# Optimization experiments

Hardware: AMD Instinct MI355X
Metric: run time of the kernel (lower is better)

## Reference

```python
import jax, jax.numpy as jnp
import numpy as np

B, N, IN_DIM, DIM, HEADS, P = 4, 2048, 256, 512, 8, 16
DH = DIM // HEADS            # 64
SCALE = DH ** -0.5


def setup_inputs() -> dict:
    key = jax.random.key(0)
    ks = jax.random.split(key, 8)
    def w(k, shape, s=0.02):
        return jax.random.normal(k, shape, dtype=jnp.float32) * s
    return {
        "x": jax.random.normal(ks[0], (B, N, IN_DIM), dtype=jnp.float32),
        "w_qkv": w(ks[1], (IN_DIM, 3 * DIM)),
        "b_qkv": jnp.zeros((3 * DIM,), jnp.float32),
        "w_in": w(ks[2], (P, P)),
        "b_in": jnp.zeros((P,), jnp.float32),
        "w_out": w(ks[3], (P, P)),
        "b_out": jnp.zeros((P,), jnp.float32),
        "w_merge": w(ks[4], (DIM, DIM)),
        "b_merge": jnp.zeros((DIM,), jnp.float32),
        "w_proj": w(ks[5], (DIM + IN_DIM, DIM)),
        "b_proj": jnp.zeros((DIM,), jnp.float32),
        "H": 64,
        "W": 32,
    }


def reference(x, w_qkv, b_qkv, w_in, b_in, w_out, b_out,
              w_merge, b_merge, w_proj, b_proj, H, W):
    b, n, _ = x.shape
    qkv = x @ w_qkv + b_qkv                      # [b, n, 3*DIM]
    q, k, v = jnp.split(qkv, 3, axis=-1)
    def to_heads(t):
        return t.reshape(b, n, HEADS, DH).transpose(0, 2, 1, 3)  # [b, h, n, d]
    q, k, v = to_heads(q), to_heads(k), to_heads(v)
    # Original splits heads into h/v halves and runs two attentions, then
    # concats along the head axis. Softmax is per-head, so this is exactly
    # one batched multi-head attention with head order preserved.
    attn = jax.nn.softmax(jnp.einsum('bhnd,bhmd->bhnm', q, k) * SCALE, axis=-1)
    out = jnp.einsum('bhnm,bhmd->bhnd', attn, v)
    out = out.transpose(0, 2, 1, 3).reshape(b, n, DIM)
    out = out @ w_merge + b_merge
    # IBPP branch: view channels as [P, P] grid, linear-SiLU-linear on last dim
    xr = x.reshape(b, n, P, P)
    ib = jax.nn.silu(xr @ w_in + b_in) @ w_out + b_out
    ib = ib.reshape(b, n, IN_DIM)
    # proj (dropout p=0 -> identity)
    return jnp.concatenate([out, ib], axis=-1) @ w_proj + b_proj
```

## Files before the change

kernel.cpp:

```cpp
#include <hip/hip_runtime.h>


typedef unsigned short u16;
typedef unsigned int u32;
typedef __bf16 bf16x8 __attribute__((ext_vector_type(8)));
typedef u16 su16x8 __attribute__((ext_vector_type(8)));
typedef u16 su16x4 __attribute__((ext_vector_type(4)));
typedef u32 u32x4 __attribute__((ext_vector_type(4)));
typedef float f32x4 __attribute__((ext_vector_type(4)));
typedef float f32x16 __attribute__((ext_vector_type(16)));

__device__ __forceinline__ u16 f2bf(float f) {
  union { __bf16 h; u16 u; } v;
  v.h = (__bf16)f;
  return v.u;
}

__device__ __forceinline__ float fexp2(float x) {
#if __has_builtin(__builtin_amdgcn_exp2f)
  return __builtin_amdgcn_exp2f(x);
#else
  return __expf(x * 0.6931471805599453f);
#endif
}

__device__ __forceinline__ f32x4 zero4() {
  f32x4 v = {0.f, 0.f, 0.f, 0.f};
  return v;
}

__device__ __forceinline__ f32x4 mfma16(bf16x8 a, bf16x8 b, f32x4 c) {
  return __builtin_amdgcn_mfma_f32_16x16x32_bf16(a, b, c, 0, 0, 0);
}

__device__ __forceinline__ f32x16 mfma32(bf16x8 a, bf16x8 b, f32x16 c) {
  return __builtin_amdgcn_mfma_f32_32x32x16_bf16(a, b, c, 0, 0, 0);
}

__device__ __forceinline__ u32 pkbf(float a, float b) {
  u32 r;
  asm("v_cvt_pk_bf16_f32 %0, %1, %2" : "=v"(r) : "v"(a), "v"(b));
  return r;
}

__device__ __forceinline__ void swap32(u32& a, u32& b) {
  asm("v_permlane32_swap_b32 %0, %1" : "+v"(a), "+v"(b));
}

__device__ __forceinline__ bf16x8 mkfrag(u32 w0, u32 w1, u32 w2, u32 w3) {
  union { u32 u[4]; bf16x8 v; } x;
  x.u[0] = w0; x.u[1] = w1; x.u[2] = w2; x.u[3] = w3;
  return x.v;
}

__global__ __launch_bounds__(256) void prep_ib_kernel(
    const float* __restrict__ w_qkv, const float* __restrict__ w_merge,
    const float* __restrict__ w_proj, const float* __restrict__ b_merge,
    const float* __restrict__ b_proj, u16* __restrict__ wqkvT,
    u16* __restrict__ wptT, u16* __restrict__ wcombT, u16* __restrict__ wmb,
    float* __restrict__ biasc, const float* __restrict__ x,
    const float* __restrict__ w_in, const float* __restrict__ b_in,
    const float* __restrict__ w_out, const float* __restrict__ b_out,
    u16* __restrict__ xb, u16* __restrict__ catb) {
  __shared__ __align__(16) char smem[35456];
  int blk = blockIdx.x, tid = threadIdx.x;
  if (blk < 192) {
    const float* src;
    int lsrc, ldd, r0, c0;
    u16* dst;
    if (blk < 96) {
      src = w_qkv; lsrc = 1536; dst = wqkvT; ldd = 256;
      r0 = (blk & 3) * 64; c0 = (blk >> 2) * 64;
    } else if (blk < 160) {
      int b2 = blk - 96;
      src = w_proj; lsrc = 512; dst = wptT; ldd = 512;
      r0 = (b2 & 7) * 64; c0 = (b2 >> 3) * 64;
    } else {
      int b2 = blk - 160;
      src = w_proj + 512 * 512; lsrc = 512; dst = wcombT + 512; ldd = 768;
      r0 = (b2 & 3) * 64; c0 = (b2 >> 2) * 64;
    }
    u16* Ts = (u16*)smem;
    int rr = tid >> 4, cc4 = (tid & 15) * 4;
#pragma unroll
    for (int rep = 0; rep < 4; ++rep) {
      int r = rr + rep * 16;
      float4 v = *(const float4*)&src[(size_t)(r0 + r) * lsrc + c0 + cc4];
      su16x4 pk = {f2bf(v.x), f2bf(v.y), f2bf(v.z), f2bf(v.w)};
      *(su16x4*)&Ts[r * 68 + cc4] = pk;
    }
    __syncthreads();
    int c = tid & 63, seg = tid >> 6;
    u16 tmp[16];
#pragma unroll
    for (int k = 0; k < 16; ++k) tmp[k] = Ts[(seg * 16 + k) * 68 + c];
    *(su16x8*)&dst[(size_t)(c0 + c) * ldd + r0 + seg * 16] = *(su16x8*)tmp;
    *(su16x8*)&dst[(size_t)(c0 + c) * ldd + r0 + seg * 16 + 8] =
        *(su16x8*)(tmp + 8);
  } else if (blk < 256) {
    int b2 = blk - 192;
#pragma unroll
    for (int rep = 0; rep < 4; ++rep) {
      int i = b2 * 4096 + rep * 1024 + tid * 4;
      float4 v = *(const float4*)&w_merge[i];
      su16x4 pk = {f2bf(v.x), f2bf(v.y), f2bf(v.z), f2bf(v.w)};
      *(su16x4*)&wmb[i] = pk;
    }
  } else if (blk < 288) {
    int col0 = (blk - 256) * 16;
    float(*red)[17] = (float(*)[17])smem;
    int kr = tid >> 4, cc = tid & 15;
    float s = 0.f;
#pragma unroll 4
    for (int j = 0; j < 32; ++j) {
      int k = kr + j * 16;
      s += b_merge[k] * w_proj[(size_t)k * 512 + col0 + cc];
    }
    red[kr][cc] = s;
    __syncthreads();
    if (kr == 0) {
      float a = b_proj[col0 + cc];
#pragma unroll
      for (int t = 0; t < 16; ++t) a += red[t][cc];
      biasc[col0 + cc] = a;
    }
  } else {
    int ib = blk - 288;
    float* wi = (float*)smem;
    float* wo = (float*)(smem + 1024);
    float* bi = (float*)(smem + 2048);
    float* bo = (float*)(smem + 2112);
    float(*xs)[260] = (float(*)[260])(smem + 2176);
    float(*hs)[260] = (float(*)[260])(smem + 18816);
    wi[tid] = w_in[tid];
    wo[tid] = w_out[tid];
    if (tid < 16) { bi[tid] = b_in[tid]; bo[tid] = b_out[tid]; }
    size_t blkoff = (size_t)ib * 4096;
#pragma unroll
    for (int i = 0; i < 4; ++i) {
      int f = (tid + i * 256) * 4;
      float4 v = *(const float4*)&x[blkoff + f];
      int tok = f >> 8, p = f & 255;
      *(float4*)&xs[tok][p] = v;
      su16x4 pk = {f2bf(v.x), f2bf(v.y), f2bf(v.z), f2bf(v.w)};
      *(su16x4*)&xb[blkoff + f] = pk;
    }
    __syncthreads();
    int t = tid >> 4, p2 = tid & 15;
#pragma unroll
    for (int p1 = 0; p1 < 16; ++p1) {
      float a = bi[p2];
#pragma unroll
      for (int k = 0; k < 16; ++k) a += xs[t][p1 * 16 + k] * wi[k * 16 + p2];
      hs[t][p1 * 16 + p2] = a / (1.f + __expf(-a));
    }
    __syncthreads();
    size_t tok = (size_t)ib * 16 + t;
#pragma unroll
    for (int p1 = 0; p1 < 16; ++p1) {
      float o = bo[p2];
#pragma unroll
      for (int j = 0; j < 16; ++j) o += hs[t][p1 * 16 + j] * wo[j * 16 + p2];
      catb[tok * 768 + 512 + p1 * 16 + p2] = f2bf(o);
    }
  }
}

template <int TM, int TN, int WGM, int WGN, int OUTMODE>
__global__ __launch_bounds__(256) void gemm_bt(
    const u16* __restrict__ A, int lda, const u16* __restrict__ BT, int ldb,
    int kcount, const float* __restrict__ bias, void* __restrict__ Co, int ldc,
    int scaleQ) {
  constexpr int NROWS = TM + TN;
  constexpr int NLD = NROWS / 64;
  constexpr int MT = TM / WGM / 16;
  constexpr int NT = TN / WGN / 16;
  __shared__ __align__(16) u16 S[NROWS * 40];
  int tid = threadIdx.x;
  int lane = tid & 63, wave = tid >> 6;
  int c = lane & 15, g4 = lane >> 4;
  int m0 = blockIdx.y * TM, n0 = blockIdx.x * TN;
  int wm = (wave / WGN) * (TM / WGM), wn = (wave % WGN) * (TN / WGN);
  f32x4 acc[MT][NT];
#pragma unroll
  for (int a = 0; a < MT; ++a)
#pragma unroll
    for (int b = 0; b < NT; ++b) acc[a][b] = zero4();

  su16x8 pre[NLD];
#pragma unroll
  for (int t = 0; t < NLD; ++t) {
    int gsl = t * 256 + tid;
    int row = gsl >> 2, kg = gsl & 3;
    const u16* p = row < TM ? &A[(size_t)(m0 + row) * lda + kg * 8]
                            : &BT[(size_t)(n0 + row - TM) * ldb + kg * 8];
    pre[t] = *(const su16x8*)p;
  }

  for (int kb = 0; kb < kcount; kb += 32) {
    __syncthreads();
#pragma unroll
    for (int t = 0; t < NLD; ++t) {
      int gsl = t * 256 + tid;
      int row = gsl >> 2, kg = gsl & 3;
      *(su16x8*)&S[row * 40 + kg * 8] = pre[t];
    }
    __syncthreads();
    if (kb + 32 < kcount) {
#pragma unroll
      for (int t = 0; t < NLD; ++t) {
        int gsl = t * 256 + tid;
        int row = gsl >> 2, kg = gsl & 3;
        const u16* p =
            row < TM ? &A[(size_t)(m0 + row) * lda + kb + 32 + kg * 8]
                     : &BT[(size_t)(n0 + row - TM) * ldb + kb + 32 + kg * 8];
        pre[t] = *(const su16x8*)p;
      }
    }
    bf16x8 af[MT], bf[NT];
#pragma unroll
    for (int mt = 0; mt < MT; ++mt)
      af[mt] = *(const bf16x8*)&S[(wm + mt * 16 + c) * 40 + g4 * 8];
#pragma unroll
    for (int nt = 0; nt < NT; ++nt)
      bf[nt] = *(const bf16x8*)&S[(TM + wn + nt * 16 + c) * 40 + g4 * 8];
#pragma unroll
    for (int mt = 0; mt < MT; ++mt)
#pragma unroll
      for (int nt = 0; nt < NT; ++nt)
        acc[mt][nt] = mfma16(af[mt], bf[nt], acc[mt][nt]);
  }

  if (OUTMODE == 0) {
    float* Cf = (float*)Co;
#pragma unroll
    for (int nt = 0; nt < NT; ++nt) {
      int col = n0 + wn + nt * 16 + c;
      float bv = bias ? bias[col] : 0.f;
#pragma unroll
      for (int mt = 0; mt < MT; ++mt)
#pragma unroll
        for (int i = 0; i < 4; ++i)
          Cf[(size_t)(m0 + wm + mt * 16 + g4 * 4 + i) * ldc + col] =
              acc[mt][nt][i] + bv;
    }
  } else if (OUTMODE == 2) {
    u16* C16 = (u16*)Co;
#pragma unroll
    for (int nt = 0; nt < NT; ++nt)
#pragma unroll
      for (int mt = 0; mt < MT; ++mt)
#pragma unroll
        for (int i = 0; i < 4; ++i)
          C16[(size_t)(m0 + wm + mt * 16 + g4 * 4 + i) * ldc + n0 + wn +
              nt * 16 + c] = f2bf(acc[mt][nt][i]);
  } else {
    u16* C16 = (u16*)Co;
    u16* Cs = S;
    __syncthreads();
#pragma unroll
    for (int half = 0; half < 2; ++half) {
      if ((wave >> 1) == half) {
#pragma unroll
        for (int nt = 0; nt < NT; ++nt) {
          int col = n0 + wn + nt * 16 + c;
          float bv = bias ? bias[col] : 0.f;
          float sc = (scaleQ && col < 512) ? 0.18033688011112042f : 1.f;
#pragma unroll
          for (int mt = 0; mt < MT; ++mt)
#pragma unroll
            for (int i = 0; i < 4; ++i)
              Cs[(mt * 16 + g4 * 4 + i) * 136 + wn + nt * 16 + c] =
                  f2bf((acc[mt][nt][i] + bv) * sc);
        }
      }
      __syncthreads();
      {
        int row = tid >> 2;
#pragma unroll
        for (int t = 0; t < 4; ++t) {
          int gr = (tid & 3) + t * 4;
          u32x4 v = *(const u32x4*)&Cs[row * 136 + gr * 8];
          *(u32x4*)&C16[(size_t)(m0 + half * 64 + row) * ldc + n0 + gr * 8] = v;
        }
      }
      __syncthreads();
    }
  }
}

__global__ __launch_bounds__(256, 2) void attn_kernel(
    const u16* __restrict__ qkvb, u16* __restrict__ catb) {
  __shared__ __align__(16) u16 Ks[2 * 9216];
  __shared__ __align__(16) u16 Vs[2 * 8704];
  int tid = threadIdx.x;
  int lane = tid & 63, wave = tid >> 6;
  int l31 = lane & 31, hi = lane >> 5;
  int qh = wave >> 1, kh = wave & 1;
  int bh = blockIdx.x & 31, qt = blockIdx.x >> 5;
  int bb = bh >> 3, h = bh & 7;
  size_t base = (size_t)bb * 2048 * 1536;

  bf16x8 qf[2][4];
#pragma unroll
  for (int qg = 0; qg < 2; ++qg) {
    int n = qt * 128 + qh * 64 + qg * 32 + l31;
    const u16* qp = &qkvb[base + (size_t)n * 1536 + h * 64 + hi * 8];
#pragma unroll
    for (int kc = 0; kc < 4; ++kc) qf[qg][kc] = *(const bf16x8*)(qp + kc * 16);
  }

  f32x16 oacc[2][2];
#pragma unroll
  for (int qg = 0; qg < 2; ++qg)
#pragma unroll
    for (int dt = 0; dt < 2; ++dt)
#pragma unroll
      for (int r = 0; r < 16; ++r) oacc[qg][dt][r] = 0.f;
  float lsum[2] = {0.f, 0.f};

  su16x8 kpre[4], v0pre[2], v1pre[2];
  int kv_s = tid >> 3, dg_s = tid & 7;

  auto loadKV = [&](int n0k) {
#pragma unroll
    for (int t = 0; t < 4; ++t)
      kpre[t] = *(const su16x8*)&qkvb[base + (size_t)(n0k + kv_s + t * 32) *
                                                1536 +
                                      512 + h * 64 + dg_s * 8];
#pragma unroll
    for (int t = 0; t < 2; ++t) {
      const u16* vg = &qkvb[base + (size_t)(n0k + (kv_s + t * 32) * 2) * 1536 +
                            1024 + h * 64 + dg_s * 8];
      v0pre[t] = *(const su16x8*)vg;
      v1pre[t] = *(const su16x8*)(vg + 1536);
    }
  };

  auto stage = [&](int buf) {
    u16* ksw = Ks + buf * 9216;
    u32* vw = (u32*)(Vs + buf * 8704);
#pragma unroll
    for (int t = 0; t < 4; ++t)
      *(su16x8*)&ksw[(kv_s + t * 32) * 72 + dg_s * 8] = kpre[t];
#pragma unroll
    for (int t = 0; t < 2; ++t) {
      int kvp = kv_s + t * 32;
      int kvg = kvp >> 2, w2 = kvp & 3;
#pragma unroll
      for (int j = 0; j < 8; ++j) {
        int d = dg_s * 8 + j;
        vw[d * 68 + ((kvg ^ (dg_s & 7)) << 2) + w2] =
            (u32)v0pre[t][j] | ((u32)v1pre[t][j] << 16);
      }
    }
  };

  loadKV(0);
  stage(0);
  for (int kb2 = 0; kb2 < 16; ++kb2) {
    __syncthreads();
    int cur = kb2 & 1;
    if (kb2 < 15) loadKV((kb2 + 1) * 128);
    const u16* ksb = Ks + cur * 9216;
    const u16* vsb = Vs + cur * 8704;
#pragma unroll
    for (int kvt = 0; kvt < 2; ++kvt) {
      bf16x8 kf[4];
#pragma unroll
      for (int kc = 0; kc < 4; ++kc)
        kf[kc] = *(const bf16x8*)&ksb[(kh * 64 + kvt * 32 + l31) * 72 +
                                      kc * 16 + hi * 8];
      f32x16 s0, s1;
#pragma unroll
      for (int r = 0; r < 16; ++r) { s0[r] = 0.f; s1[r] = 0.f; }
      __builtin_amdgcn_s_setprio(1);
#pragma unroll
      for (int kc = 0; kc < 4; ++kc) {
        s0 = mfma32(kf[kc], qf[0][kc], s0);
        s1 = mfma32(kf[kc], qf[1][kc], s1);
      }
      __builtin_amdgcn_s_setprio(0);
      bf16x8 pf[2][2];
#pragma unroll
      for (int qg = 0; qg < 2; ++qg) {
        float p[16];
#pragma unroll
        for (int r = 0; r < 16; ++r) p[r] = fexp2(qg ? s1[r] : s0[r]);
        lsum[qg] += ((((p[0] + p[1]) + (p[2] + p[3])) +
                      ((p[4] + p[5]) + (p[6] + p[7]))) +
                     (((p[8] + p[9]) + (p[10] + p[11])) +
                      ((p[12] + p[13]) + (p[14] + p[15]))));
        u32 a0 = pkbf(p[0], p[1]), b0 = pkbf(p[4], p[5]);
        u32 a1 = pkbf(p[2], p[3]), b1 = pkbf(p[6], p[7]);
        u32 a2 = pkbf(p[8], p[9]), b2 = pkbf(p[12], p[13]);
        u32 a3 = pkbf(p[10], p[11]), b3 = pkbf(p[14], p[15]);
        swap32(a0, b0);
        swap32(a1, b1);
        swap32(a2, b2);
        swap32(a3, b3);
        pf[qg][0] = mkfrag(a0, a1, b0, b1);
        pf[qg][1] = mkfrag(a2, a3, b2, b3);
      }
      __builtin_amdgcn_s_setprio(1);
#pragma unroll
      for (int kc2 = 0; kc2 < 2; ++kc2) {
        int g = kh * 8 + (kvt * 2 + kc2) * 2 + hi;
#pragma unroll
        for (int dt = 0; dt < 2; ++dt) {
          int d = dt * 32 + l31;
          bf16x8 vf =
              *(const bf16x8*)&vsb[d * 136 + ((g ^ ((d >> 3) & 7)) << 3)];
          oacc[0][dt] = mfma32(pf[0][kc2], vf, oacc[0][dt]);
          oacc[1][dt] = mfma32(pf[1][kc2], vf, oacc[1][dt]);
        }
      }
      __builtin_amdgcn_s_setprio(0);
    }
    if (kb2 < 15) stage(cur ^ 1);
  }
#pragma unroll
  for (int qg = 0; qg < 2; ++qg) lsum[qg] += __shfl_xor(lsum[qg], 32);

  __syncthreads();
  float* Of = (float*)Ks;
  float* Lf = (float*)Vs;
  if (kh == 1) {
#pragma unroll
    for (int qg = 0; qg < 2; ++qg) {
#pragma unroll
      for (int dt = 0; dt < 2; ++dt)
#pragma unroll
        for (int r = 0; r < 16; ++r) {
          int qrow = (r & 3) + 8 * (r >> 2) + 4 * hi;
          Of[(qh * 64 + qg * 32 + qrow) * 68 + dt * 32 + l31] = oacc[qg][dt][r];
        }
      if (hi == 0) Lf[qh * 64 + qg * 32 + l31] = lsum[qg];
    }
  }
  __syncthreads();
  if (kh == 0) {
#pragma unroll
    for (int qg = 0; qg < 2; ++qg) {
      float lt = lsum[qg] + Lf[qh * 64 + qg * 32 + l31];
#pragma unroll
      for (int r = 0; r < 16; ++r) {
        int qrow = (r & 3) + 8 * (r >> 2) + 4 * hi;
        float linv = 1.f / __shfl(lt, qrow);
        int qq = qh * 64 + qg * 32 + qrow;
        float o0 = oacc[qg][0][r] + Of[qq * 68 + l31];
        float o1 = oacc[qg][1][r] + Of[qq * 68 + 32 + l31];
        size_t n = (size_t)(bb * 2048 + qt * 128 + qq);
        u16* cp = &catb[n * 768 + h * 64];
        cp[l31] = f2bf(o0 * linv);
        cp[32 + l31] = f2bf(o1 * linv);
      }
    }
  }
}

extern "C" void kernel_launch(void* const* d_in, const int* in_sizes, int n_in,
                              void* d_out, int out_size, void* d_ws,
                              size_t ws_size, hipStream_t stream) {
  const float* x = (const float*)d_in[0];
  const float* w_qkv = (const float*)d_in[1];
  const float* b_qkv = (const float*)d_in[2];
  const float* w_in = (const float*)d_in[3];
  const float* b_in = (const float*)d_in[4];
  const float* w_out = (const float*)d_in[5];
  const float* b_out = (const float*)d_in[6];
  const float* w_merge = (const float*)d_in[7];
  const float* b_merge = (const float*)d_in[8];
  const float* w_proj = (const float*)d_in[9];
  const float* b_proj = (const float*)d_in[10];

  char* ws = (char*)d_ws;
  u16* xb = (u16*)(ws + 0);
  u16* qkvb = (u16*)(ws + 4194304);
  u16* catb = (u16*)(ws + 29360128);
  u16* wqkvT = (u16*)(ws + 41943040);
  u16* wptT = (u16*)(ws + 42729472);
  u16* wmb = (u16*)(ws + 43253760);
  u16* wcombT = (u16*)(ws + 43778048);
  float* biasc = (float*)(ws + 44564480);

  prep_ib_kernel<<<800, 256, 0, stream>>>(w_qkv, w_merge, w_proj, b_merge,
                                          b_proj, wqkvT, wptT, wcombT, wmb,
                                          biasc, x, w_in, b_in, w_out, b_out,
                                          xb, catb);
  gemm_bt<128, 128, 2, 2, 1><<<dim3(12, 64), 256, 0, stream>>>(
      xb, 256, wqkvT, 256, 256, b_qkv, (void*)qkvb, 1536, 1);
  gemm_bt<64, 64, 2, 2, 2><<<dim3(8, 8), 256, 0, stream>>>(
      wptT, 512, wmb, 512, 512, nullptr, (void*)wcombT, 768, 0);
  attn_kernel<<<512, 256, 0, stream>>>(qkvb, catb);
  gemm_bt<128, 64, 4, 1, 0><<<dim3(8, 64), 256, 0, stream>>>(
      catb, 768, wcombT, 768, 768, biasc, d_out, 512, 0);
}
```

Before: 182.5 us.

## Split attention KV tile across four waves per query half with tree reduction

The attention kernel moves from 256 to 512 threads per block, so each query half is served by four waves, each handling 32 keys of every 128-key tile instead of two waves handling 64. Global-to-shared staging of K/V is spread over twice as many threads, and the final partial outputs and row sums are combined with a two-level reduction through shared memory. The goal is more waves in flight to hide latency and a shorter serial chain per wave. The cost is an extra reduction stage with another barrier, larger shared memory per block, and launch bounds that ask for higher occupancy under register pressure.

```diff
diff --git a/kernel.cpp b/kernel.cpp
--- a/kernel.cpp
+++ b/kernel.cpp
@@ -289,14 +289,15 @@
   }
 }
 
-__global__ __launch_bounds__(256, 2) void attn_kernel(
+__global__ __launch_bounds__(512, 4) void attn_kernel(
     const u16* __restrict__ qkvb, u16* __restrict__ catb) {
-  __shared__ __align__(16) u16 Ks[2 * 9216];
-  __shared__ __align__(16) u16 Vs[2 * 8704];
+  __shared__ __align__(16) char smem[71680];
+  u16* Ks = (u16*)smem;
+  u16* Vs = (u16*)(smem + 36864);
   int tid = threadIdx.x;
   int lane = tid & 63, wave = tid >> 6;
   int l31 = lane & 31, hi = lane >> 5;
-  int qh = wave >> 1, kh = wave & 1;
+  int qh = wave >> 2, kh = wave & 3;
   int bh = blockIdx.x & 31, qt = blockIdx.x >> 5;
   int bb = bh >> 3, h = bh & 7;
   size_t base = (size_t)bb * 2048 * 1536;
@@ -319,21 +320,21 @@
       for (int r = 0; r < 16; ++r) oacc[qg][dt][r] = 0.f;
   float lsum[2] = {0.f, 0.f};
 
-  su16x8 kpre[4], v0pre[2], v1pre[2];
+  su16x8 kpre[2], v0pre, v1pre;
   int kv_s = tid >> 3, dg_s = tid & 7;
 
   auto loadKV = [&](int n0k) {
 #pragma unroll
-    for (int t = 0; t < 4; ++t)
-      kpre[t] = *(const su16x8*)&qkvb[base + (size_t)(n0k + kv_s + t * 32) *
+    for (int t = 0; t < 2; ++t)
+      kpre[t] = *(const su16x8*)&qkvb[base + (size_t)(n0k + kv_s + t * 64) *
                                                 1536 +
                                       512 + h * 64 + dg_s * 8];
-#pragma unroll
-    for (int t = 0; t < 2; ++t) {
-      const u16* vg = &qkvb[base + (size_t)(n0k + (kv_s + t * 32) * 2) * 1536 +
-                            1024 + h * 64 + dg_s * 8];
-      v0pre[t] = *(const su16x8*)vg;
-      v1pre[t] = *(const su16x8*)(vg + 1536);
+    {
+      const u16* vg =
+          &qkvb[base + (size_t)(n0k + kv_s * 2) * 1536 + 1024 + h * 64 +
+                dg_s * 8];
+      v0pre = *(const su16x8*)vg;
+      v1pre = *(const su16x8*)(vg + 1536);
     }
   };
 
@@ -341,17 +342,15 @@
     u16* ksw = Ks + buf * 9216;
     u32* vw = (u32*)(Vs + buf * 8704);
 #pragma unroll
-    for (int t = 0; t < 4; ++t)
-      *(su16x8*)&ksw[(kv_s + t * 32) * 72 + dg_s * 8] = kpre[t];
-#pragma unroll
-    for (int t = 0; t < 2; ++t) {
-      int kvp = kv_s + t * 32;
-      int kvg = kvp >> 2, w2 = kvp & 3;
+    for (int t = 0; t < 2; ++t)
+      *(su16x8*)&ksw[(kv_s + t * 64) * 72 + dg_s * 8] = kpre[t];
+    {
+      int kvg = kv_s >> 2, w2 = kv_s & 3;
 #pragma unroll
       for (int j = 0; j < 8; ++j) {
         int d = dg_s * 8 + j;
         vw[d * 68 + ((kvg ^ (dg_s & 7)) << 2) + w2] =
-            (u32)v0pre[t][j] | ((u32)v1pre[t][j] << 16);
+            (u32)v0pre[j] | ((u32)v1pre[j] << 16);
       }
     }
   };
@@ -364,68 +363,66 @@
     if (kb2 < 15) loadKV((kb2 + 1) * 128);
     const u16* ksb = Ks + cur * 9216;
     const u16* vsb = Vs + cur * 8704;
-#pragma unroll
-    for (int kvt = 0; kvt < 2; ++kvt) {
-      bf16x8 kf[4];
-#pragma unroll
-      for (int kc = 0; kc < 4; ++kc)
-        kf[kc] = *(const bf16x8*)&ksb[(kh * 64 + kvt * 32 + l31) * 72 +
-                                      kc * 16 + hi * 8];
-      f32x16 s0, s1;
-#pragma unroll
-      for (int r = 0; r < 16; ++r) { s0[r] = 0.f; s1[r] = 0.f; }
-      __builtin_amdgcn_s_setprio(1);
-#pragma unroll
-      for (int kc = 0; kc < 4; ++kc) {
-        s0 = mfma32(kf[kc], qf[0][kc], s0);
-        s1 = mfma32(kf[kc], qf[1][kc], s1);
-      }
-      __builtin_amdgcn_s_setprio(0);
-      bf16x8 pf[2][2];
-#pragma unroll
-      for (int qg = 0; qg < 2; ++qg) {
-        float p[16];
-#pragma unroll
-        for (int r = 0; r < 16; ++r) p[r] = fexp2(qg ? s1[r] : s0[r]);
-        lsum[qg] += ((((p[0] + p[1]) + (p[2] + p[3])) +
-                      ((p[4] + p[5]) + (p[6] + p[7]))) +
-                     (((p[8] + p[9]) + (p[10] + p[11])) +
-                      ((p[12] + p[13]) + (p[14] + p[15]))));
-        u32 a0 = pkbf(p[0], p[1]), b0 = pkbf(p[4], p[5]);
-        u32 a1 = pkbf(p[2], p[3]), b1 = pkbf(p[6], p[7]);
-        u32 a2 = pkbf(p[8], p[9]), b2 = pkbf(p[12], p[13]);
-        u32 a3 = pkbf(p[10], p[11]), b3 = pkbf(p[14], p[15]);
-        swap32(a0, b0);
-        swap32(a1, b1);
-        swap32(a2, b2);
-        swap32(a3, b3);
-        pf[qg][0] = mkfrag(a0, a1, b0, b1);
-        pf[qg][1] = mkfrag(a2, a3, b2, b3);
-      }
-      __builtin_amdgcn_s_setprio(1);
-#pragma unroll
-      for (int kc2 = 0; kc2 < 2; ++kc2) {
-        int g = kh * 8 + (kvt * 2 + kc2) * 2 + hi;
-#pragma unroll
-        for (int dt = 0; dt < 2; ++dt) {
-          int d = dt * 32 + l31;
-          bf16x8 vf =
-              *(const bf16x8*)&vsb[d * 136 + ((g ^ ((d >> 3) & 7)) << 3)];
-          oacc[0][dt] = mfma32(pf[0][kc2], vf, oacc[0][dt]);
-          oacc[1][dt] = mfma32(pf[1][kc2], vf, oacc[1][dt]);
-        }
-      }
-      __builtin_amdgcn_s_setprio(0);
-    }
+    bf16x8 kf[4];
+#pragma unroll
+    for (int kc = 0; kc < 4; ++kc)
+      kf[kc] =
+          *(const bf16x8*)&ksb[(kh * 32 + l31) * 72 + kc * 16 + hi * 8];
+    f32x16 s0, s1;
+#pragma unroll
+    for (int r = 0; r < 16; ++r) { s0[r] = 0.f; s1[r] = 0.f; }
+    __builtin_amdgcn_s_setprio(1);
+#pragma unroll
+    for (int kc = 0; kc < 4; ++kc) {
+      s0 = mfma32(kf[kc], qf[0][kc], s0);
+      s1 = mfma32(kf[kc], qf[1][kc], s1);
+    }
+    __builtin_amdgcn_s_setprio(0);
+    bf16x8 pf[2][2];
+#pragma unroll
+    for (int qg = 0; qg < 2; ++qg) {
+      float p[16];
+#pragma unroll
+      for (int r = 0; r < 16; ++r) p[r] = fexp2(qg ? s1[r] : s0[r]);
+      lsum[qg] += ((((p[0] + p[1]) + (p[2] + p[3])) +
+                    ((p[4] + p[5]) + (p[6] + p[7]))) +
+                   (((p[8] + p[9]) + (p[10] + p[11])) +
+                    ((p[12] + p[13]) + (p[14] + p[15]))));
+      u32 a0 = pkbf(p[0], p[1]), b0 = pkbf(p[4], p[5]);
+      u32 a1 = pkbf(p[2], p[3]), b1 = pkbf(p[6], p[7]);
+      u32 a2 = pkbf(p[8], p[9]), b2 = pkbf(p[12], p[13]);
+      u32 a3 = pkbf(p[10], p[11]), b3 = pkbf(p[14], p[15]);
+      swap32(a0, b0);
+      swap32(a1, b1);
+      swap32(a2, b2);
+      swap32(a3, b3);
+      pf[qg][0] = mkfrag(a0, a1, b0, b1);
+      pf[qg][1] = mkfrag(a2, a3, b2, b3);
+    }
+    __builtin_amdgcn_s_setprio(1);
+#pragma unroll
+    for (int kc2 = 0; kc2 < 2; ++kc2) {
+      int g = kh * 4 + kc2 * 2 + hi;
+#pragma unroll
+      for (int dt = 0; dt < 2; ++dt) {
+        int d = dt * 32 + l31;
+        bf16x8 vf =
+            *(const bf16x8*)&vsb[d * 136 + ((g ^ ((d >> 3) & 7)) << 3)];
+        oacc[0][dt] = mfma32(pf[0][kc2], vf, oacc[0][dt]);
+        oacc[1][dt] = mfma32(pf[1][kc2], vf, oacc[1][dt]);
+      }
+    }
+    __builtin_amdgcn_s_setprio(0);
     if (kb2 < 15) stage(cur ^ 1);
   }
 #pragma unroll
   for (int qg = 0; qg < 2; ++qg) lsum[qg] += __shfl_xor(lsum[qg], 32);
 
+  float* Of = (float*)smem;
+  float* Lf = (float*)(smem + 69632);
+  int slot = qh * 2 + (kh & 1);
   __syncthreads();
-  float* Of = (float*)Ks;
-  float* Lf = (float*)Vs;
-  if (kh == 1) {
+  if (kh >= 2) {
 #pragma unroll
     for (int qg = 0; qg < 2; ++qg) {
 #pragma unroll
@@ -433,23 +430,56 @@
 #pragma unroll
         for (int r = 0; r < 16; ++r) {
           int qrow = (r & 3) + 8 * (r >> 2) + 4 * hi;
-          Of[(qh * 64 + qg * 32 + qrow) * 68 + dt * 32 + l31] = oacc[qg][dt][r];
+          Of[(slot * 64 + qg * 32 + qrow) * 68 + dt * 32 + l31] =
+              oacc[qg][dt][r];
         }
-      if (hi == 0) Lf[qh * 64 + qg * 32 + l31] = lsum[qg];
+      if (hi == 0) Lf[slot * 64 + qg * 32 + l31] = lsum[qg];
+    }
+  }
+  __syncthreads();
+  if (kh < 2) {
+#pragma unroll
+    for (int qg = 0; qg < 2; ++qg) {
+      lsum[qg] += Lf[slot * 64 + qg * 32 + l31];
+#pragma unroll
+      for (int dt = 0; dt < 2; ++dt)
+#pragma unroll
+        for (int r = 0; r < 16; ++r) {
+          int qrow = (r & 3) + 8 * (r >> 2) + 4 * hi;
+          oacc[qg][dt][r] +=
+              Of[(slot * 64 + qg * 32 + qrow) * 68 + dt * 32 + l31];
+        }
+    }
+    if (kh == 1) {
+#pragma unroll
+      for (int qg = 0; qg < 2; ++qg) {
+#pragma unroll
+        for (int dt = 0; dt < 2; ++dt)
+#pragma unroll
+          for (int r = 0; r < 16; ++r) {
+            int qrow = (r & 3) + 8 * (r >> 2) + 4 * hi;
+            Of[(slot * 64 + qg * 32 + qrow) * 68 + dt * 32 + l31] =
+                oacc[qg][dt][r];
+          }
+        if (hi == 0) Lf[slot * 64 + qg * 32 + l31] = lsum[qg];
+      }
     }
   }
   __syncthreads();
   if (kh == 0) {
+    int oslot = qh * 2 + 1;
 #pragma unroll
     for (int qg = 0; qg < 2; ++qg) {
-      float lt = lsum[qg] + Lf[qh * 64 + qg * 32 + l31];
+      float lt = lsum[qg] + Lf[oslot * 64 + qg * 32 + l31];
 #pragma unroll
       for (int r = 0; r < 16; ++r) {
         int qrow = (r & 3) + 8 * (r >> 2) + 4 * hi;
         float linv = 1.f / __shfl(lt, qrow);
         int qq = qh * 64 + qg * 32 + qrow;
-        float o0 = oacc[qg][0][r] + Of[qq * 68 + l31];
-        float o1 = oacc[qg][1][r] + Of[qq * 68 + 32 + l31];
+        float o0 = oacc[qg][0][r] +
+                   Of[(oslot * 64 + qg * 32 + qrow) * 68 + l31];
+        float o1 = oacc[qg][1][r] +
+                   Of[(oslot * 64 + qg * 32 + qrow) * 68 + 32 + l31];
         size_t n = (size_t)(bb * 2048 + qt * 128 + qq);
         u16* cp = &catb[n * 768 + h * 64];
         cp[l31] = f2bf(o0 * linv);
@@ -492,7 +522,7 @@
       xb, 256, wqkvT, 256, 256, b_qkv, (void*)qkvb, 1536, 1);
   gemm_bt<64, 64, 2, 2, 2><<<dim3(8, 8), 256, 0, stream>>>(
       wptT, 512, wmb, 512, 512, nullptr, (void*)wcombT, 768, 0);
-  attn_kernel<<<512, 256, 0, stream>>>(qkvb, catb);
+  attn_kernel<<<512, 512, 0, stream>>>(qkvb, catb);
   gemm_bt<128, 64, 4, 1, 0><<<dim3(8, 64), 256, 0, stream>>>(
       catb, 768, wcombT, 768, 768, biasc, d_out, 512, 0);
 }
```

New measurement: 342.9 us. 1.88x slower.
